# Performance work log

Hardware: AMD Instinct MI355X
Metric: run time of the kernel (lower is better)

The kernel has to match this reference:

```python
import jax, jax.numpy as jnp
import numpy as np

N, E, G, F, H, L, NH, HD = 40000, 640000, 256, 9, 128, 3, 4, 32
EPS = 1e-5

def _ln(x, g, b):
    m = jnp.mean(x, axis=-1, keepdims=True)
    v = jnp.mean((x - m) ** 2, axis=-1, keepdims=True)
    return (x - m) * jax.lax.rsqrt(v + EPS) * g + b

def _forward(floats, edge_index, batch):
    (x, pos, emb_w, emb_b, edge_w1, edge_b1, edge_w2, edge_b2,
     node_w1, node_b1, node_w2, node_b2, qkv_w, qkv_b, out_w, out_b,
     ln1_g, ln1_b, ln2_g, ln2_b, ff_w1, ff_b1, ff_w2, ff_b2,
     cls_w1, cls_b1, cls_w2, cls_b2) = floats
    src, dst = edge_index[0], edge_index[1]  # PyG: x_j = x[src], x_i = x[dst], aggregate at dst
    dist = jnp.linalg.norm(pos[dst] - pos[src], axis=-1, keepdims=True)  # [E,1]
    h = x @ emb_w + emb_b  # [N,H]
    for l in range(L):
        # message: edge_mlp(cat[x_i, x_j, dist])
        ef = jnp.concatenate([h[dst], h[src], dist], axis=-1)  # [E,2H+1]
        m = jax.nn.silu(ef @ edge_w1[l] + edge_b1[l])
        m = jax.nn.silu(m @ edge_w2[l] + edge_b2[l])  # [E,H]
        aggr = jax.ops.segment_sum(m, dst, num_segments=N)  # [N,H]
        u = jax.nn.silu(jnp.concatenate([h, aggr], axis=-1) @ node_w1[l] + node_b1[l])
        u = u @ node_w2[l] + node_b2[l]
        h = h + u  # residual in GAHT.forward
    # per-graph mean pooling (faithful to masked-mean loop)
    sums = jax.ops.segment_sum(h, batch, num_segments=G)  # [G,H]
    cnts = jax.ops.segment_sum(jnp.ones((N,), h.dtype), batch, num_segments=G)
    g = sums / jnp.maximum(cnts, 1.0)[:, None]  # [G,H]
    # 2-layer post-norm transformer encoder (batch=1, seq=G), relu FFN, eval mode (no dropout)
    scale = 1.0 / jnp.sqrt(jnp.asarray(HD, g.dtype))
    for t in range(2):
        qkv = g @ qkv_w[t] + qkv_b[t]  # [G,3H]
        q, k, v = jnp.split(qkv, 3, axis=-1)
        q = q.reshape(G, NH, HD); k = k.reshape(G, NH, HD); v = v.reshape(G, NH, HD)
        att = jax.nn.softmax(jnp.einsum('qhd,khd->hqk', q, k) * scale, axis=-1)
        o = jnp.einsum('hqk,khd->qhd', att, v).reshape(G, H)
        o = o @ out_w[t] + out_b[t]
        g = _ln(g + o, ln1_g[t], ln1_b[t])
        ff = jax.nn.relu(g @ ff_w1[t] + ff_b1[t]) @ ff_w2[t] + ff_b2[t]
        g = _ln(g + ff, ln2_g[t], ln2_b[t])
    out = jax.nn.relu(g @ cls_w1 + cls_b1) @ cls_w2 + cls_b2  # [G,1]
    return out.squeeze(-1)  # [G]


def setup_inputs() -> dict:
    key = jax.random.key(0)
    ks = jax.random.split(key, 16)
    def p(k, shape, scale=0.08):
        return jax.random.normal(k, shape, dtype=jnp.float32) * scale
    return {
        'x': jax.random.normal(ks[0], (N, F), dtype=jnp.float32),
        'pos': jax.random.normal(ks[1], (N, 3), dtype=jnp.float32),
        'emb_w': p(ks[2], (F, H)), 'emb_b': jnp.zeros((H,), jnp.float32),
        'edge_w1': p(ks[3], (L, 2 * H + 1, H)), 'edge_b1': jnp.zeros((L, H), jnp.float32),
        'edge_w2': p(ks[4], (L, H, H)), 'edge_b2': jnp.zeros((L, H), jnp.float32),
        'node_w1': p(ks[5], (L, 2 * H, H)), 'node_b1': jnp.zeros((L, H), jnp.float32),
        'node_w2': p(ks[6], (L, H, H)), 'node_b2': jnp.zeros((L, H), jnp.float32),
        'qkv_w': p(ks[7], (2, H, 3 * H)), 'qkv_b': jnp.zeros((2, 3 * H), jnp.float32),
        'out_w': p(ks[8], (2, H, H)), 'out_b': jnp.zeros((2, H), jnp.float32),
        'ln1_g': jnp.ones((2, H), jnp.float32), 'ln1_b': jnp.zeros((2, H), jnp.float32),
        'ln2_g': jnp.ones((2, H), jnp.float32), 'ln2_b': jnp.zeros((2, H), jnp.float32),
        'ff_w1': p(ks[9], (2, H, 2 * H)), 'ff_b1': jnp.zeros((2, 2 * H), jnp.float32),
        'ff_w2': p(ks[10], (2, 2 * H, H)), 'ff_b2': jnp.zeros((2, H), jnp.float32),
        'cls_w1': p(ks[11], (H, H // 2)), 'cls_b1': jnp.zeros((H // 2,), jnp.float32),
        'cls_w2': p(ks[12], (H // 2, 1)), 'cls_b2': jnp.zeros((1,), jnp.float32),
        'edge_index': jax.random.randint(ks[13], (2, E), 0, N),
        'batch': jnp.sort(jax.random.randint(ks[14], (N,), 0, G)),
    }


def reference(x, pos, emb_w, emb_b, edge_w1, edge_b1, edge_w2, edge_b2,
              node_w1, node_b1, node_w2, node_b2, qkv_w, qkv_b, out_w, out_b,
              ln1_g, ln1_b, ln2_g, ln2_b, ff_w1, ff_b1, ff_w2, ff_b2,
              cls_w1, cls_b1, cls_w2, cls_b2, edge_index, batch):
    floats = (x, pos, emb_w, emb_b, edge_w1, edge_b1, edge_w2, edge_b2,
              node_w1, node_b1, node_w2, node_b2, qkv_w, qkv_b, out_w, out_b,
              ln1_g, ln1_b, ln2_g, ln2_b, ff_w1, ff_b1, ff_w2, ff_b2,
              cls_w1, cls_b1, cls_w2, cls_b2)
    return _forward(floats, edge_index, batch)
```

## Files before the change

### kernel.cpp

```cpp
#include <hip/hip_runtime.h>
#include <hip/hip_bf16.h>
#include <stdint.h>

#define NN 40000
#define EE 640000
#define GG 256
#define FFE 9
#define HH 128

typedef __bf16 bf16;
typedef __bf16 bf16x8 __attribute__((ext_vector_type(8)));
typedef float f32x4 __attribute__((ext_vector_type(4)));

__device__ __forceinline__ f32x4 mfma16(bf16x8 a, bf16x8 b, f32x4 c){
  return __builtin_amdgcn_mfma_f32_16x16x32_bf16(a, b, c, 0, 0, 0);
}
__device__ __forceinline__ float silu_f(float x){
  return x * __builtin_amdgcn_rcpf(1.0f + __expf(-x));
}
__device__ __forceinline__ uint16_t bfb(float x){ bf16 h=(bf16)x; return *(uint16_t*)&h; }
__device__ __forceinline__ int swz(int row, int cb){
  return row*256 + (cb ^ ((row & 7) << 4));
}

__global__ __launch_bounds__(256) void k_prep(
    const float* __restrict__ edge_w1, const float* __restrict__ edge_w2,
    const float* __restrict__ node_w1, const float* __restrict__ node_w2,
    const float* __restrict__ edge_b1,
    const float* __restrict__ x, const float* __restrict__ emb_w,
    const float* __restrict__ emb_b,
    bf16* __restrict__ wcatT, bf16* __restrict__ w2T,
    bf16* __restrict__ nw1T, bf16* __restrict__ nw2T,
    float* __restrict__ bcat, float* __restrict__ h,
    int* __restrict__ cnt)
{
  __shared__ float sx[64][9];
  __shared__ float swt[9][128];
  __shared__ float sbv[128];
  int b = blockIdx.x, tid = threadIdx.x;
  if (b < 192){
    int l = b/64; int t2 = (b%64)*256 + tid;
    int n = t2 >> 7, k = t2 & 127;
    wcatT[(size_t)l*32768 + n*128 + k] = (bf16)edge_w1[(size_t)l*32896 + k*128 + n];
  } else if (b < 384){
    int lb = b - 192; int l = lb/64; int t2 = (lb%64)*256 + tid;
    int n = t2 >> 7, k = t2 & 127;
    wcatT[(size_t)l*32768 + 16384 + n*128 + k] = (bf16)edge_w1[(size_t)l*32896 + (128+k)*128 + n];
  } else if (b < 576){
    int lb = b - 384; int l = lb/64; int t2 = (lb%64)*256 + tid;
    int n = t2 >> 7, k = t2 & 127;
    w2T[(size_t)l*16384 + n*128 + k] = (bf16)edge_w2[(size_t)l*16384 + k*128 + n];
  } else if (b < 960){
    int lb = b - 576; int l = lb/128; int t2 = (lb%128)*256 + tid;
    int n = t2 >> 8, k = t2 & 255;
    nw1T[(size_t)l*32768 + n*256 + k] = (bf16)node_w1[(size_t)l*32768 + k*128 + n];
  } else if (b < 1152){
    int lb = b - 960; int l = lb/64; int t2 = (lb%64)*256 + tid;
    int n = t2 >> 7, k = t2 & 127;
    nw2T[(size_t)l*16384 + n*128 + k] = (bf16)node_w2[(size_t)l*16384 + k*128 + n];
  } else if (b < 1155){
    int l = b - 1152;
    bcat[l*256 + tid] = (tid < 128) ? edge_b1[l*128 + tid] : 0.0f;
  } else if (b < 1312){
    int i = (b - 1155)*256 + tid;
    if (i < NN) cnt[i] = 0;
  } else {
    int m0 = (b - 1312) * 64;
    if (tid < 128) sbv[tid] = emb_b[tid];
    for (int i = tid; i < 1152; i += 256) swt[i>>7][i&127] = emb_w[i];
    for (int i = tid; i < 576; i += 256) sx[i/9][i%9] = x[(size_t)m0*9 + i];
    __syncthreads();
    int row = tid >> 2, c0 = (tid & 3) * 32;
    float xr[9];
    #pragma unroll
    for (int k=0;k<9;++k) xr[k] = sx[row][k];
    for (int j=0;j<32;j+=4){
      f32x4 a;
      #pragma unroll
      for (int r=0;r<4;++r) a[r] = sbv[c0+j+r];
      #pragma unroll
      for (int k=0;k<9;++k){
        #pragma unroll
        for (int r=0;r<4;++r) a[r] += xr[k]*swt[k][c0+j+r];
      }
      *(f32x4*)(h + (size_t)(m0+row)*128 + c0 + j) = a;
    }
  }
}

__global__ __launch_bounds__(256) void k_hist(const int* __restrict__ dst, int* __restrict__ cnt){
  int e = blockIdx.x*256 + threadIdx.x;
  if (e < EE) atomicAdd(&cnt[dst[e]], 1);
}

__global__ __launch_bounds__(1024) void k_scanA(const int* __restrict__ cnt,
    int* __restrict__ cursor, int* __restrict__ partials, int n)
{
  __shared__ int s_wsum[16];
  int tid = threadIdx.x, lane = tid & 63, wv = tid >> 6;
  int i = blockIdx.x*4096 + tid*4;
  int c0 = (i  <n)? cnt[i  ] : 0;
  int c1 = (i+1<n)? cnt[i+1] : 0;
  int c2 = (i+2<n)? cnt[i+2] : 0;
  int c3 = (i+3<n)? cnt[i+3] : 0;
  int t0 = c0, t1 = t0+c1, t2 = t1+c2, t3 = t2+c3;
  int xx = t3;
  #pragma unroll
  for (int off=1; off<64; off<<=1){ int t = __shfl_up(xx, off); if (lane>=off) xx += t; }
  if (lane==63) s_wsum[wv] = xx;
  __syncthreads();
  if (wv==0 && lane<16){
    int y = s_wsum[lane];
    #pragma unroll
    for (int off=1; off<16; off<<=1){ int t = __shfl_up(y, off, 16); if (lane>=off) y += t; }
    s_wsum[lane] = y;
  }
  __syncthreads();
  int woff = wv ? s_wsum[wv-1] : 0;
  int eb = woff + xx - t3;
  if (i  <n) cursor[i  ] = eb;
  if (i+1<n) cursor[i+1] = eb + t0;
  if (i+2<n) cursor[i+2] = eb + t1;
  if (i+3<n) cursor[i+3] = eb + t2;
  if (tid==1023) partials[blockIdx.x] = woff + xx;
}

__global__ __launch_bounds__(256) void k_scatter(
    const int* __restrict__ ei, const float* __restrict__ pos,
    int* __restrict__ cursor, const int* __restrict__ parts, int4* __restrict__ rec)
{
  __shared__ int offs_s[16];
  int tid = threadIdx.x;
  if (tid < 16){
    int v = (tid < 10) ? parts[tid] : 0;
    int xp = v;
    #pragma unroll
    for (int off=1; off<16; off<<=1){ int t = __shfl_up(xp, off, 16); if (tid>=off) xp += t; }
    offs_s[tid] = xp - v;
  }
  __syncthreads();
  int e = blockIdx.x*256 + tid;
  if (e >= EE) return;
  int s = ei[e], d = ei[EE + e];
  int p = atomicAdd(&cursor[d], 1) + offs_s[d >> 12];
  float dx = pos[d*3+0]-pos[s*3+0];
  float dy = pos[d*3+1]-pos[s*3+1];
  float dz = pos[d*3+2]-pos[s*3+2];
  int4 rc; rc.x = s; rc.y = d; rc.z = __float_as_int(sqrtf(dx*dx+dy*dy+dz*dz)); rc.w = 0;
  rec[p] = rc;
}

__global__ __launch_bounds__(256) void k_pgen(
    const float* __restrict__ h, const bf16* __restrict__ wct,
    const float* __restrict__ bcv, bf16* __restrict__ P, float* __restrict__ aggr)
{
  __shared__ bf16 SA[64][136];
  __shared__ bf16 SW[128][136];
  int tid = threadIdx.x, lane = tid & 63, w = tid >> 6;
  int rsel = lane & 15, hi = lane >> 4;
  int m0 = blockIdx.x * 64;
  f32x4 z = {0.f,0.f,0.f,0.f};
  #pragma unroll
  for (int it=0; it<8; ++it)
    *(f32x4*)(aggr + (size_t)m0*128 + (size_t)(tid + it*256)*4) = z;
  #pragma unroll
  for (int it=0; it<4; ++it){
    int idx = tid + it*256;
    int row = idx >> 4, cg = (idx & 15)*8;
    const float* sp = h + (size_t)(m0+row)*128 + cg;
    f32x4 u0 = *(const f32x4*)sp, u1v = *(const f32x4*)(sp+4);
    bf16x8 vv;
    vv[0]=(bf16)u0[0]; vv[1]=(bf16)u0[1]; vv[2]=(bf16)u0[2]; vv[3]=(bf16)u0[3];
    vv[4]=(bf16)u1v[0]; vv[5]=(bf16)u1v[1]; vv[6]=(bf16)u1v[2]; vv[7]=(bf16)u1v[3];
    *(bf16x8*)&SA[row][cg] = vv;
  }
  __syncthreads();
  int urow = w*16 + rsel;
  for (int nh=0; nh<2; ++nh){
    #pragma unroll
    for (int it=0; it<8; ++it){
      int idx = tid + it*256;
      int row = idx >> 4, cg = (idx & 15)*8;
      *(bf16x8*)&SW[row][cg] = *(const bf16x8*)(wct + (size_t)(nh*128+row)*128 + cg);
    }
    __syncthreads();
    f32x4 acc[8];
    #pragma unroll
    for (int nt=0;nt<8;++nt)
      #pragma unroll
      for (int r=0;r<4;++r) acc[nt][r]=0.f;
    #pragma unroll
    for (int ks=0; ks<4; ++ks){
      int kb = ks*32 + hi*8;
      bf16x8 fa = *(const bf16x8*)&SA[urow][kb];
      #pragma unroll
      for (int nt=0;nt<8;++nt){
        bf16x8 fw = *(const bf16x8*)&SW[nt*16 + rsel][kb];
        acc[nt] = mfma16(fw, fa, acc[nt]);
      }
    }
    __syncthreads();
    #pragma unroll
    for (int nt=0;nt<8;++nt){
      int nb = nh*128 + nt*16 + 4*hi;
      f32x4 b4 = *(const f32x4*)(bcv + nb);
      uint2 pk;
      pk.x = (unsigned)bfb(acc[nt][0] + b4[0]) | ((unsigned)bfb(acc[nt][1] + b4[1]) << 16);
      pk.y = (unsigned)bfb(acc[nt][2] + b4[2]) | ((unsigned)bfb(acc[nt][3] + b4[3]) << 16);
      *(uint2*)(P + (size_t)(m0+urow)*256 + nb) = pk;
    }
  }
}

template<bool DOP>
__global__ __launch_bounds__(512) void k_node(
    float* h, float* aggr,
    const bf16* __restrict__ nw1t,
    const bf16* __restrict__ nw2t,
    const bf16* __restrict__ wct,
    const float* __restrict__ nb1, const float* __restrict__ nb2,
    const float* __restrict__ bcv,
    bf16* __restrict__ P)
{
  __shared__ bf16 SA[64][68];
  __shared__ bf16 SW[128][72];
  __shared__ bf16 SU[64][132];
  __shared__ bf16 SH[64][132];
  int tid = threadIdx.x, lane = tid & 63, w = tid >> 6;
  int rsel = lane & 15, hi = lane >> 4;
  int m0 = blockIdx.x * 64;
  int nbase = w*16 + 4*hi;

  f32x4 acc[4];
  #pragma unroll
  for (int rt=0;rt<4;++rt)
    #pragma unroll
    for (int r=0;r<4;++r) acc[rt][r]=0.f;

  for (int kq=0; kq<4; ++kq){
    const float* src = (kq < 2) ? (h + (size_t)m0*128 + kq*64)
                                : (aggr + (size_t)m0*128 + (kq-2)*64);
    {
      int g = tid, row = g >> 3, cg = (g & 7)*8;
      const float* sp = src + (size_t)row*128 + cg;
      f32x4 u0 = *(const f32x4*)sp, u1v = *(const f32x4*)(sp+4);
      bf16x8 vv;
      vv[0]=(bf16)u0[0]; vv[1]=(bf16)u0[1]; vv[2]=(bf16)u0[2]; vv[3]=(bf16)u0[3];
      vv[4]=(bf16)u1v[0]; vv[5]=(bf16)u1v[1]; vv[6]=(bf16)u1v[2]; vv[7]=(bf16)u1v[3];
      *(bf16x8*)&SA[row][cg] = vv;
    }
    #pragma unroll
    for (int it=0; it<2; ++it){
      int g = tid + it*512, row = g >> 3, cg = (g & 7)*8;
      *(bf16x8*)&SW[row][cg] = *(const bf16x8*)(nw1t + (size_t)row*256 + kq*64 + cg);
    }
    __syncthreads();
    #pragma unroll
    for (int ks=0; ks<2; ++ks){
      int kb = ks*32 + hi*8;
      bf16x8 fw = *(const bf16x8*)&SW[w*16 + rsel][kb];
      #pragma unroll
      for (int rt=0; rt<4; ++rt){
        bf16x8 fa = *(const bf16x8*)&SA[rt*16 + rsel][kb];
        acc[rt] = mfma16(fw, fa, acc[rt]);
      }
    }
    __syncthreads();
  }

  {
    f32x4 b4 = *(const f32x4*)(nb1 + nbase);
    #pragma unroll
    for (int rt=0; rt<4; ++rt){
      uint2 pk;
      pk.x = (unsigned)bfb(silu_f(acc[rt][0]+b4[0])) | ((unsigned)bfb(silu_f(acc[rt][1]+b4[1]))<<16);
      pk.y = (unsigned)bfb(silu_f(acc[rt][2]+b4[2])) | ((unsigned)bfb(silu_f(acc[rt][3]+b4[3]))<<16);
      *(uint2*)&SU[rt*16 + rsel][nbase] = pk;
    }
  }

  #pragma unroll
  for (int rt=0;rt<4;++rt)
    #pragma unroll
    for (int r=0;r<4;++r) acc[rt][r]=0.f;
  for (int kq=0; kq<2; ++kq){
    #pragma unroll
    for (int it=0; it<2; ++it){
      int g = tid + it*512, row = g >> 3, cg = (g & 7)*8;
      *(bf16x8*)&SW[row][cg] = *(const bf16x8*)(nw2t + (size_t)row*128 + kq*64 + cg);
    }
    __syncthreads();
    #pragma unroll
    for (int ks=0; ks<2; ++ks){
      int kb = ks*32 + hi*8;
      bf16x8 fw = *(const bf16x8*)&SW[w*16 + rsel][kb];
      #pragma unroll
      for (int rt=0; rt<4; ++rt){
        bf16x8 fa = *(const bf16x8*)&SU[rt*16 + rsel][kq*64 + kb];
        acc[rt] = mfma16(fw, fa, acc[rt]);
      }
    }
    __syncthreads();
  }

  {
    f32x4 c4 = *(const f32x4*)(nb2 + nbase);
    #pragma unroll
    for (int rt=0; rt<4; ++rt){
      int grow = m0 + rt*16 + rsel;
      f32x4 h4 = *(const f32x4*)(h + (size_t)grow*128 + nbase);
      f32x4 v;
      #pragma unroll
      for (int r=0;r<4;++r) v[r] = h4[r] + acc[rt][r] + c4[r];
      *(f32x4*)(h + (size_t)grow*128 + nbase) = v;
      uint2 pk;
      pk.x = (unsigned)bfb(v[0]) | ((unsigned)bfb(v[1]) << 16);
      pk.y = (unsigned)bfb(v[2]) | ((unsigned)bfb(v[3]) << 16);
      *(uint2*)&SH[rt*16 + rsel][nbase] = pk;
    }
  }

  if (DOP){
    for (int nh=0; nh<2; ++nh){
      f32x4 a3[4];
      #pragma unroll
      for (int rt=0;rt<4;++rt)
        #pragma unroll
        for (int r=0;r<4;++r) a3[rt][r]=0.f;
      for (int kq=0; kq<2; ++kq){
        #pragma unroll
        for (int it=0; it<2; ++it){
          int g = tid + it*512, row = g >> 3, cg = (g & 7)*8;
          *(bf16x8*)&SW[row][cg] = *(const bf16x8*)(wct + (size_t)(nh*128+row)*128 + kq*64 + cg);
        }
        __syncthreads();
        #pragma unroll
        for (int ks=0; ks<2; ++ks){
          int kb = ks*32 + hi*8;
          bf16x8 fw = *(const bf16x8*)&SW[w*16 + rsel][kb];
          #pragma unroll
          for (int rt=0; rt<4; ++rt){
            bf16x8 fa = *(const bf16x8*)&SH[rt*16 + rsel][kq*64 + kb];
            a3[rt] = mfma16(fw, fa, a3[rt]);
          }
        }
        __syncthreads();
      }
      f32x4 bb4 = *(const f32x4*)(bcv + nh*128 + nbase);
      #pragma unroll
      for (int rt=0; rt<4; ++rt){
        int grow = m0 + rt*16 + rsel;
        uint2 pk;
        pk.x = (unsigned)bfb(a3[rt][0]+bb4[0]) | ((unsigned)bfb(a3[rt][1]+bb4[1])<<16);
        pk.y = (unsigned)bfb(a3[rt][2]+bb4[2]) | ((unsigned)bfb(a3[rt][3]+bb4[3])<<16);
        *(uint2*)(P + (size_t)grow*256 + nh*128 + nbase) = pk;
      }
    }
    f32x4 z = {0.f,0.f,0.f,0.f};
    #pragma unroll
    for (int it=0; it<4; ++it)
      *(f32x4*)(aggr + (size_t)m0*128 + (size_t)(tid + it*512)*4) = z;
  }
}

__global__ __launch_bounds__(512, 6) void k_edge(
    const bf16* __restrict__ P, const bf16* __restrict__ w2t,
    const float* __restrict__ w1r, const float* __restrict__ b2,
    const int4* __restrict__ rec, float* __restrict__ aggr)
{
  __shared__ char smem[32768];
  __shared__ int s_dst[128];
  __shared__ int s_segid[128];
  __shared__ int s_segdst[128];
  __shared__ bf16 s_sel[16][136];
  __shared__ int s_misc[4];
  int tid = threadIdx.x, lane = tid & 63, w = tid >> 6;
  int rsel = lane & 15, hi = lane >> 4;
  int bid = blockIdx.x;
  int swb = (bid & 7) * (EE/128/8) + (bid >> 3);
  int e0 = swb * 128;
  int col = w*16 + rsel;

  bf16x8 fb[4];
  #pragma unroll
  for (int ks=0;ks<4;++ks)
    fb[ks] = *(const bf16x8*)(w2t + (size_t)col*128 + ks*32 + hi*8);

  if (tid == 0){
    s_misc[0] = (e0 == 0) ? -2147483647 : rec[e0-1].y;
    s_misc[1] = (e0 + 128 >= EE) ? -2147483647 : rec[e0+128].y;
  }

  int cq = (tid & 15)*8;
  int er = tid >> 4;
  int4 rc[4];
  #pragma unroll
  for (int it=0; it<4; ++it) rc[it] = rec[e0 + er + it*32];
  uint4 pau[4], pbu[4];
  #pragma unroll
  for (int it=0; it<4; ++it){
    pau[it] = *(const uint4*)(P + ((size_t)rc[it].y << 8) + cq);
    pbu[it] = *(const uint4*)(P + ((size_t)rc[it].x << 8) + 128 + cq);
  }
  if (cq == 0){
    #pragma unroll
    for (int it=0; it<4; ++it) s_dst[er + it*32] = rc[it].y;
  }
  f32x4 wr0 = *(const f32x4*)(w1r + cq);
  f32x4 wr1 = *(const f32x4*)(w1r + cq + 4);
  #pragma unroll
  for (int it=0; it<4; ++it){
    float dist = __int_as_float(rc[it].z);
    bf16x8 mm;
    #pragma unroll
    for (int j=0;j<4;++j){
      unsigned ua = ((const unsigned*)&pau[it])[j];
      unsigned ub = ((const unsigned*)&pbu[it])[j];
      float al = __uint_as_float(ua << 16);
      float ah = __uint_as_float(ua & 0xFFFF0000u);
      float bl = __uint_as_float(ub << 16);
      float bh = __uint_as_float(ub & 0xFFFF0000u);
      float wlo = (j<2) ? wr0[2*j]   : wr1[2*(j-2)];
      float whi = (j<2) ? wr0[2*j+1] : wr1[2*(j-2)+1];
      mm[2*j]   = (bf16)silu_f(al + bl + dist*wlo);
      mm[2*j+1] = (bf16)silu_f(ah + bh + dist*whi);
    }
    *(bf16x8*)(smem + swz(er + it*32, cq*2)) = mm;
  }
  __syncthreads();

  if (w == 0){
    int d0 = s_dst[2*lane], d1 = s_dst[2*lane+1];
    int dm1 = (lane == 0) ? 0 : s_dst[2*lane-1];
    int h0 = (lane == 0) ? 1 : (d0 != dm1);
    int h1 = (d1 != d0);
    int p = h0 + h1, x = p;
    #pragma unroll
    for (int off=1; off<64; off<<=1){ int t = __shfl_up(x, off); if (lane>=off) x += t; }
    int excl = x - p;
    int id0 = excl + h0 - 1;
    int id1 = excl + p - 1;
    s_segid[2*lane]   = id0;
    s_segid[2*lane+1] = id1;
    if (h0) s_segdst[id0] = d0;
    if (h1) s_segdst[id1] = d1;
    if (lane == 63) s_misc[2] = id1 + 1;
  }

  f32x4 acc[8];
  #pragma unroll
  for (int mt=0;mt<8;++mt)
    #pragma unroll
    for (int r=0;r<4;++r) acc[mt][r]=0.f;
  #pragma unroll
  for (int mt=0;mt<8;++mt){
    #pragma unroll
    for (int ks=0;ks<4;++ks){
      bf16x8 fa = *(const bf16x8*)(smem + swz(mt*16 + rsel, ks*64 + hi*16));
      acc[mt] = mfma16(fa, fb[ks], acc[mt]);
    }
  }
  __syncthreads();

  float bb = b2[col];
  #pragma unroll
  for (int mt=0;mt<8;++mt){
    uint2 pk;
    pk.x = (unsigned)bfb(silu_f(acc[mt][0] + bb)) | ((unsigned)bfb(silu_f(acc[mt][1] + bb)) << 16);
    pk.y = (unsigned)bfb(silu_f(acc[mt][2] + bb)) | ((unsigned)bfb(silu_f(acc[mt][3] + bb)) << 16);
    *(uint2*)(smem + col*256 + ((mt*32 + hi*8) ^ ((col & 7) << 4))) = pk;
  }
  __syncthreads();

  bf16x8 gb[4];
  #pragma unroll
  for (int ks=0;ks<4;++ks)
    gb[ks] = *(const bf16x8*)(smem + col*256 + ((ks*64 + hi*16) ^ ((col & 7) << 4)));
  int nseg = s_misc[2];
  bool openL = (s_dst[0]   == s_misc[0]);
  bool openR = (s_dst[127] == s_misc[1]);
  const bf16 ONE = (bf16)1.0f, ZERO = (bf16)0.0f;
  for (int st = 0; st < nseg; st += 16){
    __syncthreads();
    #pragma unroll
    for (int k4=0;k4<4;++k4){
      int idx = tid + k4*512;
      int s = idx >> 7, e = idx & 127;
      s_sel[s][e] = (s_segid[e] == st + s) ? ONE : ZERO;
    }
    __syncthreads();
    f32x4 racc = {0.f,0.f,0.f,0.f};
    #pragma unroll
    for (int ks=0;ks<4;++ks){
      bf16x8 sa = *(const bf16x8*)&s_sel[rsel][ks*32 + hi*8];
      racc = mfma16(sa, gb[ks], racc);
    }
    #pragma unroll
    for (int r=0;r<4;++r){
      int s = st + 4*hi + r;
      if (s < nseg){
        float v = racc[r];
        size_t off = (size_t)s_segdst[s]*128 + col;
        bool atom = (s == 0 && openL) || (s == nseg-1 && openR);
        if (atom) atomicAdd(&aggr[off], v);
        else      aggr[off] = v;
      }
    }
  }
}

__device__ __forceinline__ int lbound(const int* a, int n, int key){
  int lo=0, hi=n;
  while (lo<hi){ int mid=(lo+hi)>>1; if (a[mid]<key) lo=mid+1; else hi=mid; }
  return lo;
}

__global__ __launch_bounds__(384) void k_pool_qkv(
    const float* __restrict__ h, const int* __restrict__ batch,
    const float* __restrict__ wq, const float* __restrict__ bq,
    float* __restrict__ gbuf, float* __restrict__ qkvb)
{
  __shared__ float sg[128];
  int gr = blockIdx.x, tid = threadIdx.x;
  if (tid < 128){
    int lo = lbound(batch, NN, gr), hi2 = lbound(batch, NN, gr+1);
    float s = 0.f;
    for (int n=lo;n<hi2;++n) s += h[(size_t)n*HH + tid];
    int c = hi2 - lo; if (c < 1) c = 1;
    s /= (float)c;
    sg[tid] = s; gbuf[gr*128 + tid] = s;
  }
  __syncthreads();
  float a = bq[tid];
  for (int k=0;k<128;++k) a += sg[k]*wq[k*384 + tid];
  qkvb[gr*384 + tid] = a;
}

template<int MODE>
__global__ __launch_bounds__(128) void k_tail(
    const float* __restrict__ qkv, const float* __restrict__ wo,
    const float* __restrict__ bo, const float* __restrict__ l1g,
    const float* __restrict__ l1b, const float* __restrict__ w1,
    const float* __restrict__ b1f, const float* __restrict__ w2,
    const float* __restrict__ b2f, const float* __restrict__ l2g,
    const float* __restrict__ l2b, float* __restrict__ gbuf,
    const float* __restrict__ wq2, const float* __restrict__ bq2,
    float* __restrict__ qkvb2,
    const float* __restrict__ cw1, const float* __restrict__ cb1,
    const float* __restrict__ cw2, const float* __restrict__ cb2,
    float* __restrict__ out)
{
  __shared__ float sq[128];
  __shared__ float ss[4][256];
  __shared__ float so[128];
  __shared__ float st[256];
  __shared__ float red[4];
  int r = blockIdx.x, tid = threadIdx.x;
  sq[tid] = qkv[r*384 + tid];
  __syncthreads();
  const float scale = 0.17677669529663687f;
  for (int i=tid; i<1024; i+=128){
    int hh = i >> 8, j = i & 255;
    const float* kr = qkv + j*384 + 128 + hh*32;
    const float* qr = sq + hh*32;
    float s=0;
    #pragma unroll
    for (int d=0;d<32;++d) s += qr[d]*kr[d];
    ss[hh][j] = s*scale;
  }
  __syncthreads();
  int hh = tid >> 5, sl = tid & 31;
  float m = -1e30f;
  #pragma unroll
  for (int q8=0;q8<8;++q8) m = fmaxf(m, ss[hh][sl + q8*32]);
  #pragma unroll
  for (int off=16; off; off>>=1) m = fmaxf(m, __shfl_xor(m, off, 32));
  float sum = 0.f;
  #pragma unroll
  for (int q8=0;q8<8;++q8){
    float e = __expf(ss[hh][sl+q8*32] - m);
    ss[hh][sl+q8*32] = e;
    sum += e;
  }
  #pragma unroll
  for (int off=16; off; off>>=1) sum += __shfl_xor(sum, off, 32);
  float inv = __builtin_amdgcn_rcpf(sum);
  __syncthreads();
  float accv = 0.f;
  for (int j=0;j<256;++j) accv += ss[hh][j]*qkv[j*384 + 256 + hh*32 + sl];
  so[tid] = accv*inv;
  __syncthreads();
  float a = bo[tid];
  for (int k=0;k<128;++k) a += so[k]*wo[k*128 + tid];
  float val = gbuf[r*128 + tid] + a;
  {
    float s = val, q = val*val;
    #pragma unroll
    for (int off=32; off; off>>=1){ s += __shfl_xor(s, off); q += __shfl_xor(q, off); }
    int lane = tid & 63, wv = tid >> 6;
    if (lane==0){ red[wv*2]=s; red[wv*2+1]=q; }
    __syncthreads();
    float S = red[0]+red[2], Q = red[1]+red[3];
    float mean = S*(1.0f/128.0f);
    float var = Q*(1.0f/128.0f) - mean*mean;
    float ninv = rsqrtf(var + 1e-5f);
    val = (val-mean)*ninv*l1g[tid] + l1b[tid];
  }
  sq[tid] = val;
  __syncthreads();
  float a0 = b1f[tid], a1 = b1f[tid+128];
  for (int k=0;k<128;++k){
    float gv = sq[k];
    a0 += gv*w1[k*256 + tid];
    a1 += gv*w1[k*256 + tid + 128];
  }
  st[tid]     = fmaxf(a0, 0.f);
  st[tid+128] = fmaxf(a1, 0.f);
  __syncthreads();
  float b = b2f[tid];
  for (int k=0;k<256;++k) b += st[k]*w2[k*128 + tid];
  float val2 = val + b;
  {
    float s = val2, q = val2*val2;
    #pragma unroll
    for (int off=32; off; off>>=1){ s += __shfl_xor(s, off); q += __shfl_xor(q, off); }
    int lane = tid & 63, wv = tid >> 6;
    __syncthreads();
    if (lane==0){ red[wv*2]=s; red[wv*2+1]=q; }
    __syncthreads();
    float S = red[0]+red[2], Q = red[1]+red[3];
    float mean = S*(1.0f/128.0f);
    float var = Q*(1.0f/128.0f) - mean*mean;
    float ninv = rsqrtf(var + 1e-5f);
    val2 = (val2-mean)*ninv*l2g[tid] + l2b[tid];
  }
  gbuf[r*128 + tid] = val2;
  if (MODE == 0){
    sq[tid] = val2;
    __syncthreads();
    float q0 = bq2[tid], q1 = bq2[tid+128], q2 = bq2[tid+256];
    for (int k=0;k<128;++k){
      float gv = sq[k];
      const float* wr = wq2 + k*384;
      q0 += gv*wr[tid]; q1 += gv*wr[tid+128]; q2 += gv*wr[tid+256];
    }
    qkvb2[r*384+tid]=q0; qkvb2[r*384+tid+128]=q1; qkvb2[r*384+tid+256]=q2;
  }
  if (MODE == 1){
    so[tid] = val2;
    __syncthreads();
    if (tid < 64){
      float c = cb1[tid];
      for (int k=0;k<128;++k) c += so[k]*cw1[k*64 + tid];
      c = fmaxf(c, 0.f);
      float p = c * cw2[tid];
      #pragma unroll
      for (int off=32; off; off>>=1) p += __shfl_xor(p, off);
      if (tid==0) out[r] = p + cb2[0];
    }
  }
}

extern "C" void kernel_launch(void* const* d_in, const int* in_sizes, int n_in,
                              void* d_out, int out_size, void* d_ws, size_t ws_size,
                              hipStream_t stream)
{
  (void)in_sizes; (void)n_in; (void)out_size; (void)ws_size;
  const float* x      = (const float*)d_in[0];
  const float* pos    = (const float*)d_in[1];
  const float* emb_w  = (const float*)d_in[2];
  const float* emb_b  = (const float*)d_in[3];
  const float* edge_w1= (const float*)d_in[4];
  const float* edge_b1= (const float*)d_in[5];
  const float* edge_w2= (const float*)d_in[6];
  const float* edge_b2= (const float*)d_in[7];
  const float* node_w1= (const float*)d_in[8];
  const float* node_b1= (const float*)d_in[9];
  const float* node_w2= (const float*)d_in[10];
  const float* node_b2= (const float*)d_in[11];
  const float* qkv_w  = (const float*)d_in[12];
  const float* qkv_b  = (const float*)d_in[13];
  const float* out_w  = (const float*)d_in[14];
  const float* out_b  = (const float*)d_in[15];
  const float* ln1_g  = (const float*)d_in[16];
  const float* ln1_b  = (const float*)d_in[17];
  const float* ln2_g  = (const float*)d_in[18];
  const float* ln2_b  = (const float*)d_in[19];
  const float* ff_w1  = (const float*)d_in[20];
  const float* ff_b1  = (const float*)d_in[21];
  const float* ff_w2  = (const float*)d_in[22];
  const float* ff_b2  = (const float*)d_in[23];
  const float* cls_w1 = (const float*)d_in[24];
  const float* cls_b1 = (const float*)d_in[25];
  const float* cls_w2 = (const float*)d_in[26];
  const float* cls_b2 = (const float*)d_in[27];
  const int* ei       = (const int*)d_in[28];
  const int* batch    = (const int*)d_in[29];
  float* out = (float*)d_out;

  uint8_t* wp = (uint8_t*)d_ws;
  auto take = [&](size_t nb)->void*{ void* r = wp; wp += (nb + 255) & ~(size_t)255; return r; };
  float* h      = (float*)take((size_t)NN*HH*4);
  bf16*  P      = (bf16*) take((size_t)NN*256*2);
  float* aggr   = (float*)take((size_t)NN*HH*4);
  int*   cnt    = (int*)  take((size_t)NN*4);
  int*   cursor = (int*)  take((size_t)NN*4);
  int*   parts  = (int*)  take((size_t)64*4);
  int4*  rec    = (int4*) take((size_t)EE*16);
  bf16*  wcatT  = (bf16*) take((size_t)3*256*128*2);
  bf16*  w2T    = (bf16*) take((size_t)3*128*128*2);
  bf16*  nw1T   = (bf16*) take((size_t)3*128*256*2);
  bf16*  nw2T   = (bf16*) take((size_t)3*128*128*2);
  float* bcat   = (float*)take((size_t)3*256*4);
  float* gbuf   = (float*)take((size_t)GG*HH*4);
  float* qkvb   = (float*)take((size_t)GG*384*4);
  float* qkvb2  = (float*)take((size_t)GG*384*4);

  dim3 b256(256);
  k_prep<<<dim3(1937), b256, 0, stream>>>(edge_w1, edge_w2, node_w1, node_w2,
    edge_b1, x, emb_w, emb_b, wcatT, w2T, nw1T, nw2T, bcat, h, cnt);
  k_hist<<<dim3(EE/256), b256, 0, stream>>>(ei + EE, cnt);
  k_scanA<<<dim3(10), dim3(1024), 0, stream>>>(cnt, cursor, parts, NN);
  k_scatter<<<dim3(EE/256), b256, 0, stream>>>(ei, pos, cursor, parts, rec);

  k_pgen<<<dim3(625), b256, 0, stream>>>(h, wcatT, bcat, P, aggr);

  for (int l=0;l<3;++l){
    k_edge<<<dim3(EE/128), dim3(512), 0, stream>>>(P, w2T + (size_t)l*16384,
      edge_w1 + ((size_t)l*257 + 256)*128, edge_b2 + (size_t)l*128, rec, aggr);
    if (l < 2){
      k_node<true><<<dim3(625), dim3(512), 0, stream>>>(h, aggr,
        nw1T + (size_t)l*32768, nw2T + (size_t)l*16384, wcatT + (size_t)(l+1)*32768,
        node_b1 + (size_t)l*128, node_b2 + (size_t)l*128, bcat + (size_t)(l+1)*256, P);
    } else {
      k_node<false><<<dim3(625), dim3(512), 0, stream>>>(h, aggr,
        nw1T + (size_t)l*32768, nw2T + (size_t)l*16384, wcatT,
        node_b1 + (size_t)l*128, node_b2 + (size_t)l*128, bcat, P);
    }
  }

  k_pool_qkv<<<dim3(GG), dim3(384), 0, stream>>>(h, batch, qkv_w, qkv_b, gbuf, qkvb);
  k_tail<0><<<dim3(GG), dim3(128), 0, stream>>>(qkvb, out_w, out_b,
    ln1_g, ln1_b, ff_w1, ff_b1, ff_w2, ff_b2, ln2_g, ln2_b, gbuf,
    qkv_w + (size_t)128*384, qkv_b + 384, qkvb2,
    nullptr, nullptr, nullptr, nullptr, nullptr);
  k_tail<1><<<dim3(GG), dim3(128), 0, stream>>>(qkvb2, out_w + (size_t)128*128, out_b + 128,
    ln1_g + 128, ln1_b + 128, ff_w1 + (size_t)128*256, ff_b1 + 256,
    ff_w2 + (size_t)256*128, ff_b2 + 128, ln2_g + 128, ln2_b + 128, gbuf,
    nullptr, nullptr, nullptr,
    cls_w1, cls_b1, cls_w2, cls_b2, out);
}
```

Before: 629.1 us.

## Fuse layer-0 projection into embedding prep kernel and unroll tail loops

Removes the separate k_pgen launch by computing the layer-0 edge projection P and zeroing aggr inside the embedding blocks of k_prep. The embedded h is kept in shared memory as bf16, and the edge_w1 weights are read and transposed directly from fp32 global memory, so the kernel no longer waits on a separate transposed-weight pass. The aim is to save one launch and one round trip of h through global memory. The cost is uncoalesced strided weight reads and much larger shared memory use in k_prep, which may lower occupancy for all its blocks. It also splits accumulators and unrolls loops in the pooling and transformer tail kernels, and adds a barrier in k_node.

```diff
diff --git a/kernel.cpp b/kernel.cpp
--- a/kernel.cpp
+++ b/kernel.cpp
@@ -32,11 +32,14 @@
     bf16* __restrict__ wcatT, bf16* __restrict__ w2T,
     bf16* __restrict__ nw1T, bf16* __restrict__ nw2T,
     float* __restrict__ bcat, float* __restrict__ h,
-    int* __restrict__ cnt)
+    int* __restrict__ cnt, bf16* __restrict__ P, float* __restrict__ aggr)
 {
-  __shared__ float sx[64][9];
-  __shared__ float swt[9][128];
-  __shared__ float sbv[128];
+  __shared__ char SM[59648];
+  bf16 (*SW)[138] = (bf16(*)[138])SM;
+  bf16 (*SH)[132] = (bf16(*)[132])(SM + 35328);
+  float (*sx)[9]  = (float(*)[9]) (SM + 52224);
+  float (*swt)[128]=(float(*)[128])(SM + 54528);
+  float* sbv      = (float*)      (SM + 59136);
   int b = blockIdx.x, tid = threadIdx.x;
   if (b < 192){
     int l = b/64; int t2 = (b%64)*256 + tid;
@@ -66,24 +69,79 @@
     if (i < NN) cnt[i] = 0;
   } else {
     int m0 = (b - 1312) * 64;
+    int lane = tid & 63, w = tid >> 6;
+    int rsel = lane & 15, hi = lane >> 4;
+    f32x4 z = {0.f,0.f,0.f,0.f};
+    #pragma unroll
+    for (int it=0; it<8; ++it)
+      *(f32x4*)(aggr + (size_t)m0*128 + (size_t)(tid + it*256)*4) = z;
     if (tid < 128) sbv[tid] = emb_b[tid];
     for (int i = tid; i < 1152; i += 256) swt[i>>7][i&127] = emb_w[i];
     for (int i = tid; i < 576; i += 256) sx[i/9][i%9] = x[(size_t)m0*9 + i];
     __syncthreads();
-    int row = tid >> 2, c0 = (tid & 3) * 32;
-    float xr[9];
-    #pragma unroll
-    for (int k=0;k<9;++k) xr[k] = sx[row][k];
-    for (int j=0;j<32;j+=4){
-      f32x4 a;
-      #pragma unroll
-      for (int r=0;r<4;++r) a[r] = sbv[c0+j+r];
-      #pragma unroll
-      for (int k=0;k<9;++k){
+    {
+      int row = tid >> 2, c0 = (tid & 3) * 32;
+      float xr[9];
+      #pragma unroll
+      for (int k=0;k<9;++k) xr[k] = sx[row][k];
+      #pragma unroll
+      for (int j=0;j<32;j+=4){
+        f32x4 a;
         #pragma unroll
-        for (int r=0;r<4;++r) a[r] += xr[k]*swt[k][c0+j+r];
-      }
-      *(f32x4*)(h + (size_t)(m0+row)*128 + c0 + j) = a;
+        for (int r=0;r<4;++r) a[r] = sbv[c0+j+r];
+        #pragma unroll
+        for (int k=0;k<9;++k){
+          #pragma unroll
+          for (int r=0;r<4;++r) a[r] += xr[k]*swt[k][c0+j+r];
+        }
+        *(f32x4*)(h + (size_t)(m0+row)*128 + c0 + j) = a;
+        uint2 pk;
+        pk.x = (unsigned)bfb(a[0]) | ((unsigned)bfb(a[1]) << 16);
+        pk.y = (unsigned)bfb(a[2]) | ((unsigned)bfb(a[3]) << 16);
+        *(uint2*)&SH[row][c0+j] = pk;
+      }
+    }
+    __syncthreads();
+    int urow = w*16 + rsel;
+    for (int nh=0; nh<2; ++nh){
+      #pragma unroll
+      for (int it=0; it<8; ++it){
+        int t = it*256 + tid;
+        int n = t & 127, k0 = (t >> 7) * 8;
+        bf16x8 vv;
+        #pragma unroll
+        for (int j=0;j<8;++j)
+          vv[j] = (bf16)edge_w1[(size_t)(nh*128 + k0 + j)*128 + n];
+        *(bf16x8*)&SW[n][k0] = vv;
+      }
+      __syncthreads();
+      f32x4 acc[8];
+      #pragma unroll
+      for (int nt=0;nt<8;++nt)
+        #pragma unroll
+        for (int r=0;r<4;++r) acc[nt][r]=0.f;
+      #pragma unroll
+      for (int ks=0; ks<4; ++ks){
+        int kb = ks*32 + hi*8;
+        bf16x8 fa = *(const bf16x8*)&SH[urow][kb];
+        #pragma unroll
+        for (int nt=0;nt<8;++nt){
+          bf16x8 fw = *(const bf16x8*)&SW[nt*16 + rsel][kb];
+          acc[nt] = mfma16(fw, fa, acc[nt]);
+        }
+      }
+      __syncthreads();
+      #pragma unroll
+      for (int nt=0;nt<8;++nt){
+        int nb = nt*16 + 4*hi;
+        f32x4 b4;
+        if (nh == 0) b4 = *(const f32x4*)(edge_b1 + nb);
+        else { b4[0]=0.f; b4[1]=0.f; b4[2]=0.f; b4[3]=0.f; }
+        uint2 pk;
+        pk.x = (unsigned)bfb(acc[nt][0] + b4[0]) | ((unsigned)bfb(acc[nt][1] + b4[1]) << 16);
+        pk.y = (unsigned)bfb(acc[nt][2] + b4[2]) | ((unsigned)bfb(acc[nt][3] + b4[3]) << 16);
+        *(uint2*)(P + (size_t)(m0+urow)*256 + nh*128 + nb) = pk;
+      }
     }
   }
 }
@@ -148,68 +206,6 @@
   float dz = pos[d*3+2]-pos[s*3+2];
   int4 rc; rc.x = s; rc.y = d; rc.z = __float_as_int(sqrtf(dx*dx+dy*dy+dz*dz)); rc.w = 0;
   rec[p] = rc;
-}
-
-__global__ __launch_bounds__(256) void k_pgen(
-    const float* __restrict__ h, const bf16* __restrict__ wct,
-    const float* __restrict__ bcv, bf16* __restrict__ P, float* __restrict__ aggr)
-{
-  __shared__ bf16 SA[64][136];
-  __shared__ bf16 SW[128][136];
-  int tid = threadIdx.x, lane = tid & 63, w = tid >> 6;
-  int rsel = lane & 15, hi = lane >> 4;
-  int m0 = blockIdx.x * 64;
-  f32x4 z = {0.f,0.f,0.f,0.f};
-  #pragma unroll
-  for (int it=0; it<8; ++it)
-    *(f32x4*)(aggr + (size_t)m0*128 + (size_t)(tid + it*256)*4) = z;
-  #pragma unroll
-  for (int it=0; it<4; ++it){
-    int idx = tid + it*256;
-    int row = idx >> 4, cg = (idx & 15)*8;
-    const float* sp = h + (size_t)(m0+row)*128 + cg;
-    f32x4 u0 = *(const f32x4*)sp, u1v = *(const f32x4*)(sp+4);
-    bf16x8 vv;
-    vv[0]=(bf16)u0[0]; vv[1]=(bf16)u0[1]; vv[2]=(bf16)u0[2]; vv[3]=(bf16)u0[3];
-    vv[4]=(bf16)u1v[0]; vv[5]=(bf16)u1v[1]; vv[6]=(bf16)u1v[2]; vv[7]=(bf16)u1v[3];
-    *(bf16x8*)&SA[row][cg] = vv;
-  }
-  __syncthreads();
-  int urow = w*16 + rsel;
-  for (int nh=0; nh<2; ++nh){
-    #pragma unroll
-    for (int it=0; it<8; ++it){
-      int idx = tid + it*256;
-      int row = idx >> 4, cg = (idx & 15)*8;
-      *(bf16x8*)&SW[row][cg] = *(const bf16x8*)(wct + (size_t)(nh*128+row)*128 + cg);
-    }
-    __syncthreads();
-    f32x4 acc[8];
-    #pragma unroll
-    for (int nt=0;nt<8;++nt)
-      #pragma unroll
-      for (int r=0;r<4;++r) acc[nt][r]=0.f;
-    #pragma unroll
-    for (int ks=0; ks<4; ++ks){
-      int kb = ks*32 + hi*8;
-      bf16x8 fa = *(const bf16x8*)&SA[urow][kb];
-      #pragma unroll
-      for (int nt=0;nt<8;++nt){
-        bf16x8 fw = *(const bf16x8*)&SW[nt*16 + rsel][kb];
-        acc[nt] = mfma16(fw, fa, acc[nt]);
-      }
-    }
-    __syncthreads();
-    #pragma unroll
-    for (int nt=0;nt<8;++nt){
-      int nb = nh*128 + nt*16 + 4*hi;
-      f32x4 b4 = *(const f32x4*)(bcv + nb);
-      uint2 pk;
-      pk.x = (unsigned)bfb(acc[nt][0] + b4[0]) | ((unsigned)bfb(acc[nt][1] + b4[1]) << 16);
-      pk.y = (unsigned)bfb(acc[nt][2] + b4[2]) | ((unsigned)bfb(acc[nt][3] + b4[3]) << 16);
-      *(uint2*)(P + (size_t)(m0+urow)*256 + nb) = pk;
-    }
-  }
 }
 
 template<bool DOP>
@@ -321,6 +317,7 @@
   }
 
   if (DOP){
+    __syncthreads();
     for (int nh=0; nh<2; ++nh){
       f32x4 a3[4];
       #pragma unroll
@@ -524,14 +521,23 @@
   int gr = blockIdx.x, tid = threadIdx.x;
   if (tid < 128){
     int lo = lbound(batch, NN, gr), hi2 = lbound(batch, NN, gr+1);
-    float s = 0.f;
-    for (int n=lo;n<hi2;++n) s += h[(size_t)n*HH + tid];
+    float s0=0.f, s1=0.f, s2=0.f, s3=0.f;
+    int n = lo;
+    for (; n+3<hi2; n+=4){
+      s0 += h[(size_t)n*HH + tid];
+      s1 += h[(size_t)(n+1)*HH + tid];
+      s2 += h[(size_t)(n+2)*HH + tid];
+      s3 += h[(size_t)(n+3)*HH + tid];
+    }
+    for (; n<hi2; ++n) s0 += h[(size_t)n*HH + tid];
+    float s = (s0+s1)+(s2+s3);
     int c = hi2 - lo; if (c < 1) c = 1;
     s /= (float)c;
     sg[tid] = s; gbuf[gr*128 + tid] = s;
   }
   __syncthreads();
   float a = bq[tid];
+  #pragma unroll 4
   for (int k=0;k<128;++k) a += sg[k]*wq[k*384 + tid];
   qkvb[gr*384 + tid] = a;
 }
@@ -586,11 +592,16 @@
   for (int off=16; off; off>>=1) sum += __shfl_xor(sum, off, 32);
   float inv = __builtin_amdgcn_rcpf(sum);
   __syncthreads();
-  float accv = 0.f;
-  for (int j=0;j<256;++j) accv += ss[hh][j]*qkv[j*384 + 256 + hh*32 + sl];
-  so[tid] = accv*inv;
+  float av0 = 0.f, av1 = 0.f;
+  #pragma unroll 4
+  for (int j=0;j<256;j+=2){
+    av0 += ss[hh][j]*qkv[j*384 + 256 + hh*32 + sl];
+    av1 += ss[hh][j+1]*qkv[(j+1)*384 + 256 + hh*32 + sl];
+  }
+  so[tid] = (av0+av1)*inv;
   __syncthreads();
   float a = bo[tid];
+  #pragma unroll 4
   for (int k=0;k<128;++k) a += so[k]*wo[k*128 + tid];
   float val = gbuf[r*128 + tid] + a;
   {
@@ -609,6 +620,7 @@
   sq[tid] = val;
   __syncthreads();
   float a0 = b1f[tid], a1 = b1f[tid+128];
+  #pragma unroll 4
   for (int k=0;k<128;++k){
     float gv = sq[k];
     a0 += gv*w1[k*256 + tid];
@@ -618,6 +630,7 @@
   st[tid+128] = fmaxf(a1, 0.f);
   __syncthreads();
   float b = b2f[tid];
+  #pragma unroll 4
   for (int k=0;k<256;++k) b += st[k]*w2[k*128 + tid];
   float val2 = val + b;
   {
@@ -639,6 +652,7 @@
     sq[tid] = val2;
     __syncthreads();
     float q0 = bq2[tid], q1 = bq2[tid+128], q2 = bq2[tid+256];
+    #pragma unroll 4
     for (int k=0;k<128;++k){
       float gv = sq[k];
       const float* wr = wq2 + k*384;
@@ -651,6 +665,7 @@
     __syncthreads();
     if (tid < 64){
       float c = cb1[tid];
+      #pragma unroll 4
       for (int k=0;k<128;++k) c += so[k]*cw1[k*64 + tid];
       c = fmaxf(c, 0.f);
       float p = c * cw2[tid];
@@ -718,12 +733,10 @@
 
   dim3 b256(256);
   k_prep<<<dim3(1937), b256, 0, stream>>>(edge_w1, edge_w2, node_w1, node_w2,
-    edge_b1, x, emb_w, emb_b, wcatT, w2T, nw1T, nw2T, bcat, h, cnt);
+    edge_b1, x, emb_w, emb_b, wcatT, w2T, nw1T, nw2T, bcat, h, cnt, P, aggr);
   k_hist<<<dim3(EE/256), b256, 0, stream>>>(ei + EE, cnt);
   k_scanA<<<dim3(10), dim3(1024), 0, stream>>>(cnt, cursor, parts, NN);
   k_scatter<<<dim3(EE/256), b256, 0, stream>>>(ei, pos, cursor, parts, rec);
-
-  k_pgen<<<dim3(625), b256, 0, stream>>>(h, wcatT, bcat, P, aggr);
 
   for (int l=0;l<3;++l){
     k_edge<<<dim3(EE/128), dim3(512), 0, stream>>>(P, w2T + (size_t)l*16384,
```

New measurement: 671.2 us. 6.7% more time.
